# Performance work log

Measured on AMD Instinct MI355X. Metric: run time of the kernel, lower is better.

Reference implementation:

```python
import jax, jax.numpy as jnp
import numpy as np

B = 1024        # number of graphs in the batch
D = 256         # per-type node feature dim
DG = 128        # global (direct-cat) feature dim
N_ATOM = 65536
N_BOND = 131072
N_ITERS = 6


def _lstm_step(q_star, h, c, W_ih, W_hh, b_ih, b_hh):
    # torch LSTM gate order: i, f, g, o
    gates = q_star @ W_ih.T + b_ih + h @ W_hh.T + b_hh  # [B, 4D]
    i, f, g, o = jnp.split(gates, 4, axis=-1)
    c = jax.nn.sigmoid(f) * c + jax.nn.sigmoid(i) * jnp.tanh(g)
    h = jax.nn.sigmoid(o) * jnp.tanh(c)
    return h, c


def _set2set(feat, seg, W_ih, W_hh, b_ih, b_hh, n_iters, batch_size):
    d = feat.shape[1]
    h = jnp.zeros((batch_size, d), feat.dtype)
    c = jnp.zeros((batch_size, d), feat.dtype)
    q_star = jnp.zeros((batch_size, 2 * d), feat.dtype)
    for _ in range(n_iters):
        h, c = _lstm_step(q_star, h, c, W_ih, W_hh, b_ih, b_hh)
        q = h  # [B, D]
        # per-node attention logit: e_i = x_i . q_{seg(i)}
        e = jnp.sum(feat * q[seg], axis=-1)  # [N]
        # segment softmax (stable)
        m = jax.ops.segment_max(e, seg, num_segments=batch_size)
        ex = jnp.exp(e - m[seg])
        denom = jax.ops.segment_sum(ex, seg, num_segments=batch_size)
        alpha = ex / denom[seg]  # [N]
        # weighted readout per graph
        r = jax.ops.segment_sum(feat * alpha[:, None], seg, num_segments=batch_size)  # [B, D]
        q_star = jnp.concatenate([q, r], axis=-1)
    return q_star  # [B, 2D]


def setup_inputs() -> dict:
    key = jax.random.key(0)
    ks = jax.random.split(key, 12)
    s = 1.0 / np.sqrt(D)  # torch LSTM init range
    inp = {
        "feat_atom": jax.random.normal(ks[0], (N_ATOM, D), jnp.float32),
        "seg_atom": (jnp.arange(N_ATOM) // (N_ATOM // B)).astype(jnp.int32),
        "feat_bond": jax.random.normal(ks[1], (N_BOND, D), jnp.float32),
        "seg_bond": (jnp.arange(N_BOND) // (N_BOND // B)).astype(jnp.int32),
        "feat_global": jax.random.normal(ks[2], (B, DG), jnp.float32),
        "W_ih_atom": jax.random.uniform(ks[3], (4 * D, 2 * D), jnp.float32, -s, s),
        "W_hh_atom": jax.random.uniform(ks[4], (4 * D, D), jnp.float32, -s, s),
        "b_ih_atom": jax.random.uniform(ks[5], (4 * D,), jnp.float32, -s, s),
        "b_hh_atom": jax.random.uniform(ks[6], (4 * D,), jnp.float32, -s, s),
        "W_ih_bond": jax.random.uniform(ks[7], (4 * D, 2 * D), jnp.float32, -s, s),
        "W_hh_bond": jax.random.uniform(ks[8], (4 * D, D), jnp.float32, -s, s),
        "b_ih_bond": jax.random.uniform(ks[9], (4 * D,), jnp.float32, -s, s),
        "b_hh_bond": jax.random.uniform(ks[10], (4 * D,), jnp.float32, -s, s),
    }
    return inp


def reference(feat_atom, seg_atom, feat_bond, seg_bond, feat_global,
              W_ih_atom, W_hh_atom, b_ih_atom, b_hh_atom,
              W_ih_bond, W_hh_bond, b_ih_bond, b_hh_bond):
    qa = _set2set(feat_atom, seg_atom, W_ih_atom, W_hh_atom, b_ih_atom, b_hh_atom, N_ITERS, B)
    qb = _set2set(feat_bond, seg_bond, W_ih_bond, W_hh_bond, b_ih_bond, b_hh_bond, N_ITERS, B)
    return jnp.concatenate([qa, qb, feat_global], axis=-1)  # [B, 2D + 2D + DG]
```

## Files before the change

kernel.cpp:

```cpp
#include <hip/hip_runtime.h>
#include <stdint.h>

#define NGRAPH 1024
#define DFEAT  256
#define KATOM  64
#define KBOND  128

typedef __attribute__((ext_vector_type(4))) float accv_t;
typedef __attribute__((ext_vector_type(8))) short bfrag_t;
typedef __attribute__((ext_vector_type(4))) unsigned short upk4_t;
typedef __attribute__((ext_vector_type(8))) unsigned short upk8_t;
typedef __attribute__((ext_vector_type(4))) unsigned int u32x4;

__device__ __forceinline__ unsigned short f2bf(float f) {
    union { float f; unsigned int u; } v; v.f = f;
    return (unsigned short)((v.u + 0x7FFFu + ((v.u >> 16) & 1u)) >> 16);
}
__device__ __forceinline__ float sigm(float x) { return 1.0f / (1.0f + __expf(-x)); }
__device__ __forceinline__ float tanh_f(float x) {
    float e = __expf(2.0f * x);
    return 1.0f - 2.0f / (e + 1.0f);
}

__global__ __launch_bounds__(256) void k_cvt(
    const float* __restrict__ fA, const float* __restrict__ fB,
    unsigned int* __restrict__ oA, unsigned int* __restrict__ oB,
    float* __restrict__ scA, float* __restrict__ scB)
{
    int wid  = blockIdx.x * 4 + (threadIdx.x >> 6);
    int lane = threadIdx.x & 63;
    int grp  = lane >> 3;

    #pragma unroll 2
    for (int n = wid; n < 65536; n += 4096) {
        accv_t v = __builtin_nontemporal_load((const accv_t*)(fA + (size_t)n * 256) + lane);
        float m = fmaxf(fmaxf(fabsf(v[0]), fabsf(v[1])), fmaxf(fabsf(v[2]), fabsf(v[3])));
        m = fmaxf(m, __shfl_xor(m, 1));
        m = fmaxf(m, __shfl_xor(m, 2));
        m = fmaxf(m, __shfl_xor(m, 4));
        float inv = (m > 0.0f) ? 127.0f / m : 0.0f;
        int q0 = (int)rintf(v[0] * inv), q1 = (int)rintf(v[1] * inv);
        int q2 = (int)rintf(v[2] * inv), q3 = (int)rintf(v[3] * inv);
        oA[(size_t)n * 64 + lane] = (unsigned int)(q0 & 0xFF) | ((unsigned int)(q1 & 0xFF) << 8)
                                  | ((unsigned int)(q2 & 0xFF) << 16) | ((unsigned int)(q3 & 0xFF) << 24);
        if ((lane & 7) == 0) scA[(size_t)n * 8 + grp] = m * (1.0f / 127.0f);
    }
    #pragma unroll 2
    for (int n = wid; n < 131072; n += 4096) {
        accv_t v = __builtin_nontemporal_load((const accv_t*)(fB + (size_t)n * 256) + lane);
        float m = fmaxf(fmaxf(fabsf(v[0]), fabsf(v[1])), fmaxf(fabsf(v[2]), fabsf(v[3])));
        m = fmaxf(m, __shfl_xor(m, 1));
        m = fmaxf(m, __shfl_xor(m, 2));
        m = fmaxf(m, __shfl_xor(m, 4));
        float inv = (m > 0.0f) ? 127.0f / m : 0.0f;
        int q0 = (int)rintf(v[0] * inv), q1 = (int)rintf(v[1] * inv);
        int q2 = (int)rintf(v[2] * inv), q3 = (int)rintf(v[3] * inv);
        oB[(size_t)n * 64 + lane] = (unsigned int)(q0 & 0xFF) | ((unsigned int)(q1 & 0xFF) << 8)
                                  | ((unsigned int)(q2 & 0xFF) << 16) | ((unsigned int)(q3 & 0xFF) << 24);
        if ((lane & 7) == 0) scB[(size_t)n * 8 + grp] = m * (1.0f / 127.0f);
    }
}

__global__ __launch_bounds__(512) void k_prep(
    const float* __restrict__ WihA, const float* __restrict__ WhhA,
    const float* __restrict__ bihA, const float* __restrict__ bhhA,
    const float* __restrict__ WihB, const float* __restrict__ WhhB,
    const float* __restrict__ bihB, const float* __restrict__ bhhB,
    unsigned short* __restrict__ Wc, float* __restrict__ bsum)
{
    int bid = blockIdx.x;
    int set = bid >> 10;
    int n   = bid & 1023;
    int k   = threadIdx.x;
    const float* Wih = set ? WihB : WihA;
    const float* Whh = set ? WhhB : WhhA;
    float w = Wih[(size_t)n * 512 + k];
    if (k < 256) w += Whh[(size_t)n * 256 + k];
    Wc[((size_t)(set << 10) + n) * 512 + k] = f2bf(w);
    if (k == 0) {
        const float* bih = set ? bihB : bihA;
        const float* bhh = set ? bhhB : bhhA;
        bsum[(set << 10) + n] = bih[n] + bhh[n];
    }
}

__global__ __launch_bounds__(256) void k_gemm(
    const float* __restrict__ hr, const unsigned short* __restrict__ Wc,
    const float* __restrict__ bsum, float* __restrict__ gates)
{
    __shared__ unsigned short sA[64 * 40];
    __shared__ unsigned short sB[128 * 40];

    int set   = blockIdx.x >> 7;
    int qq    = blockIdx.x & 127;
    int mbase = (qq >> 3) * 64;
    int nbase = (qq & 7) * 128;
    int t     = threadIdx.x;
    int lane  = t & 63;
    int w     = t >> 6;
    int wrow  = (w >> 1) * 32;
    int wcol  = (w & 1) * 64;
    int l15   = lane & 15;
    int khalf = (lane >> 4) * 8;

    const float* A           = hr + (size_t)(set << 10) * 512;
    const unsigned short* Bm = Wc + (size_t)(set << 10) * 512;

    accv_t acc[2][4];
    #pragma unroll
    for (int i = 0; i < 2; ++i)
        #pragma unroll
        for (int j = 0; j < 4; ++j)
            acc[i][j] = (accv_t){0.f, 0.f, 0.f, 0.f};

    for (int k0 = 0; k0 < 512; k0 += 32) {
        #pragma unroll
        for (int i = 0; i < 2; ++i) {
            int idx4 = t + 256 * i;
            int row  = idx4 >> 3;
            int kc   = (idx4 & 7) * 4;
            const float4 a = *(const float4*)&A[(size_t)(mbase + row) * 512 + k0 + kc];
            upk4_t u;
            u[0] = f2bf(a.x); u[1] = f2bf(a.y); u[2] = f2bf(a.z); u[3] = f2bf(a.w);
            *(upk4_t*)&sA[row * 40 + kc] = u;
        }
        #pragma unroll
        for (int i = 0; i < 2; ++i) {
            int idx8 = t + 256 * i;
            int row  = idx8 >> 2;
            int kc   = (idx8 & 3) * 8;
            *(upk8_t*)&sB[row * 40 + kc] =
                *(const upk8_t*)&Bm[(size_t)(nbase + row) * 512 + k0 + kc];
        }
        __syncthreads();

        bfrag_t a_f[2], b_f[4];
        #pragma unroll
        for (int i = 0; i < 2; ++i)
            a_f[i] = *(const bfrag_t*)&sA[(wrow + i * 16 + l15) * 40 + khalf];
        #pragma unroll
        for (int j = 0; j < 4; ++j)
            b_f[j] = *(const bfrag_t*)&sB[(wcol + j * 16 + l15) * 40 + khalf];
        #pragma unroll
        for (int i = 0; i < 2; ++i)
            #pragma unroll
            for (int j = 0; j < 4; ++j)
                acc[i][j] = __builtin_amdgcn_mfma_f32_16x16x32_bf16(a_f[i], b_f[j], acc[i][j], 0, 0, 0);
        __syncthreads();
    }

    int r4 = (lane >> 4) * 4;
    #pragma unroll
    for (int i = 0; i < 2; ++i) {
        #pragma unroll
        for (int j = 0; j < 4; ++j) {
            int col  = nbase + wcol + j * 16 + l15;
            float bs = bsum[(set << 10) + col];
            #pragma unroll
            for (int v = 0; v < 4; ++v) {
                int row = mbase + wrow + i * 16 + r4 + v;
                gates[((size_t)(set << 10) + row) * 1024 + col] = acc[i][j][v] + bs;
            }
        }
    }
}

template <int MODE, bool LAST>
__global__ __launch_bounds__(256) void k_attn(
    const float* __restrict__ featA, const float* __restrict__ featB,
    const unsigned int* __restrict__ i8A, const unsigned int* __restrict__ i8B,
    const float* __restrict__ scA, const float* __restrict__ scB,
    const float* __restrict__ gates, const float* __restrict__ bsum,
    float* __restrict__ hr, float* __restrict__ cst,
    const float* __restrict__ fgp, float* __restrict__ outp, int iter)
{
    __shared__ float qv[256];
    __shared__ float sw_s[16], cw_s[16];
    __shared__ float racc_s[16][260];

    int bid = blockIdx.x;
    int set = (bid < 1024) ? 1 : 0;
    int b   = bid & 1023;
    int K   = set ? KBOND : KATOM;
    int t = threadIdx.x;
    size_t sb = (size_t)(set << 10) + b;
    size_t ob = (size_t)b * 1152 + (set ? 512 : 0);

    {
        int d = t;
        float gi, gf, gg, go, cold;
        if (iter == 0) {
            gi = bsum[(set << 10) + d];
            gf = bsum[(set << 10) + 256 + d];
            gg = bsum[(set << 10) + 512 + d];
            go = bsum[(set << 10) + 768 + d];
            cold = 0.0f;
        } else {
            const float* gp = gates + sb * 1024;
            gi = gp[d]; gf = gp[256 + d]; gg = gp[512 + d]; go = gp[768 + d];
            cold = cst[sb * 256 + d];
        }
        float cn = sigm(gf) * cold + sigm(gi) * tanh_f(gg);
        float h  = sigm(go) * tanh_f(cn);
        if (LAST) { outp[ob + d] = h; }
        else      { cst[sb * 256 + d] = cn; hr[sb * 512 + d] = h; }
        qv[d] = h;
    }
    __syncthreads();

    int lane = t & 63;
    int wv   = t >> 6;
    int g    = lane >> 4;
    int s    = lane & 15;
    int npw  = K >> 2;
    int nq   = npw >> 2;
    int node0 = wv * npw + g;
    float C = 0.0f, sacc = 0.0f;
    int pid = (wv << 2) | g;

    if (MODE == 1) {
        const unsigned int* fb = (set ? i8B : i8A)
                               + ((size_t)b * K + node0) * 64 + s * 4;
        const float* scp = (set ? scB : scA)
                         + ((size_t)b * K + node0) * 8 + (s >> 1);

        float qr[16];
        #pragma unroll
        for (int j = 0; j < 16; ++j) qr[j] = qv[s * 16 + j];
        float r[16];
        #pragma unroll
        for (int j = 0; j < 16; ++j) r[j] = 0.0f;

        #pragma unroll 4
        for (int qd = 0; qd < nq; ++qd) {
            u32x4 hx = *(const u32x4*)(fb + (size_t)qd * 256);
            float sc = scp[(size_t)qd * 32];
            float x[16];
            #pragma unroll
            for (int w4 = 0; w4 < 4; ++w4) {
                unsigned int u = hx[w4];
                x[w4 * 4 + 0] = (float)((int)(u << 24) >> 24);
                x[w4 * 4 + 1] = (float)((int)(u << 16) >> 24);
                x[w4 * 4 + 2] = (float)((int)(u << 8)  >> 24);
                x[w4 * 4 + 3] = (float)((int)u >> 24);
            }
            float e = 0.0f;
            #pragma unroll
            for (int j = 0; j < 16; ++j) e += x[j] * qr[j];
            e *= sc;
            e += __shfl_xor(e, 1);
            e += __shfl_xor(e, 2);
            e += __shfl_xor(e, 4);
            e += __shfl_xor(e, 8);
            float w = (qd == 0) ? 1.0f : __expf(e - C);
            if (qd == 0) C = e;
            sacc += w;
            float wl = w * sc;
            #pragma unroll
            for (int j = 0; j < 16; ++j) r[j] += wl * x[j];
        }
        #pragma unroll
        for (int j = 0; j < 16; j += 4)
            *(float4*)&racc_s[pid][s * 16 + j] = *(float4*)&r[j];
    } else {
        const float* feat = set ? featB : featA;
        const float* fb = feat + ((size_t)b * K + node0) * 256 + s * 4;
        float4 q0 = *(const float4*)&qv[s*4];
        float4 q1 = *(const float4*)&qv[64  + s*4];
        float4 q2 = *(const float4*)&qv[128 + s*4];
        float4 q3 = *(const float4*)&qv[192 + s*4];
        float4 r0 = make_float4(0.f,0.f,0.f,0.f), r1 = r0, r2 = r0, r3 = r0;
        #pragma unroll 2
        for (int qd = 0; qd < nq; ++qd) {
            const float* p = fb + (size_t)qd * 1024;
            float4 x0 = *(const float4*)(p);
            float4 x1 = *(const float4*)(p + 64);
            float4 x2 = *(const float4*)(p + 128);
            float4 x3 = *(const float4*)(p + 192);
            float e = x0.x*q0.x + x0.y*q0.y + x0.z*q0.z + x0.w*q0.w
                    + x1.x*q1.x + x1.y*q1.y + x1.z*q1.z + x1.w*q1.w
                    + x2.x*q2.x + x2.y*q2.y + x2.z*q2.z + x2.w*q2.w
                    + x3.x*q3.x + x3.y*q3.y + x3.z*q3.z + x3.w*q3.w;
            e += __shfl_xor(e, 1); e += __shfl_xor(e, 2);
            e += __shfl_xor(e, 4); e += __shfl_xor(e, 8);
            float w = (qd == 0) ? 1.0f : __expf(e - C);
            if (qd == 0) C = e;
            sacc += w;
            r0.x += w*x0.x; r0.y += w*x0.y; r0.z += w*x0.z; r0.w += w*x0.w;
            r1.x += w*x1.x; r1.y += w*x1.y; r1.z += w*x1.z; r1.w += w*x1.w;
            r2.x += w*x2.x; r2.y += w*x2.y; r2.z += w*x2.z; r2.w += w*x2.w;
            r3.x += w*x3.x; r3.y += w*x3.y; r3.z += w*x3.z; r3.w += w*x3.w;
        }
        *(float4*)&racc_s[pid][s*4]       = r0;
        *(float4*)&racc_s[pid][64  + s*4] = r1;
        *(float4*)&racc_s[pid][128 + s*4] = r2;
        *(float4*)&racc_s[pid][192 + s*4] = r3;
    }
    if (s == 0) { sw_s[pid] = sacc; cw_s[pid] = C; }
    __syncthreads();

    {
        float Cm = cw_s[0];
        #pragma unroll
        for (int p2 = 1; p2 < 16; ++p2) Cm = fmaxf(Cm, cw_s[p2]);
        float S = 0.0f, r = 0.0f;
        #pragma unroll
        for (int p2 = 0; p2 < 16; ++p2) {
            float f = __expf(cw_s[p2] - Cm);
            S += sw_s[p2] * f;
            r += racc_s[p2][t] * f;
        }
        float rv = r / S;
        if (LAST) {
            outp[ob + 256 + t] = rv;
            if (set && t < 128)
                outp[(size_t)b * 1152 + 1024 + t] = fgp[(size_t)b * 128 + t];
        } else {
            hr[sb * 512 + 256 + t] = rv;
        }
    }
}

__global__ __launch_bounds__(288) void k_out(
    const float* __restrict__ hr, const float* __restrict__ fg,
    float* __restrict__ out)
{
    int b  = blockIdx.x;
    int c4 = threadIdx.x * 4;
    float4 v;
    if (c4 < 512)       v = *(const float4*)&hr[(size_t)b * 512 + c4];
    else if (c4 < 1024) v = *(const float4*)&hr[(size_t)(1024 + b) * 512 + (c4 - 512)];
    else                v = *(const float4*)&fg[(size_t)b * 128 + (c4 - 1024)];
    *(float4*)&out[(size_t)b * 1152 + c4] = v;
}

extern "C" void kernel_launch(void* const* d_in, const int* in_sizes, int n_in,
                              void* d_out, int out_size, void* d_ws, size_t ws_size,
                              hipStream_t stream) {
    const float* feat_atom   = (const float*)d_in[0];
    const float* feat_bond   = (const float*)d_in[2];
    const float* feat_global = (const float*)d_in[4];
    const float* WihA = (const float*)d_in[5];
    const float* WhhA = (const float*)d_in[6];
    const float* bihA = (const float*)d_in[7];
    const float* bhhA = (const float*)d_in[8];
    const float* WihB = (const float*)d_in[9];
    const float* WhhB = (const float*)d_in[10];
    const float* bihB = (const float*)d_in[11];
    const float* bhhB = (const float*)d_in[12];
    float* out = (float*)d_out;

    char* ws = (char*)d_ws;
    unsigned short* Wc = (unsigned short*)(ws + 0);
    float* bsum  = (float*)(ws + 2097152);
    float* gates = (float*)(ws + 2105344);
    float* hr    = (float*)(ws + 10493952);
    float* cst   = (float*)(ws + 14688256);
    unsigned int* i8A = (unsigned int*)(ws + 16785408);
    unsigned int* i8B = (unsigned int*)(ws + 33562624);
    float* scA = (float*)(ws + 67117056);
    float* scB = (float*)(ws + 69214208);
    const size_t WS_NEED = 69214208 + 4194304;
    (void)in_sizes; (void)n_in; (void)out_size;

    bool i8 = (ws_size >= WS_NEED);

    k_prep<<<2048, 512, 0, stream>>>(WihA, WhhA, bihA, bhhA,
                                     WihB, WhhB, bihB, bhhB, Wc, bsum);
    if (i8) {
        k_cvt<<<1024, 256, 0, stream>>>(feat_atom, feat_bond, i8A, i8B, scA, scB);
        k_attn<1, false><<<2048, 256, 0, stream>>>(feat_atom, feat_bond, i8A, i8B,
                                                   scA, scB, gates, bsum, hr, cst,
                                                   feat_global, out, 0);
        for (int it = 1; it < 5; ++it) {
            k_gemm<<<256, 256, 0, stream>>>(hr, Wc, bsum, gates);
            k_attn<1, false><<<2048, 256, 0, stream>>>(feat_atom, feat_bond, i8A, i8B,
                                                       scA, scB, gates, bsum, hr, cst,
                                                       feat_global, out, it);
        }
        k_gemm<<<256, 256, 0, stream>>>(hr, Wc, bsum, gates);
        k_attn<1, true><<<2048, 256, 0, stream>>>(feat_atom, feat_bond, i8A, i8B,
                                                  scA, scB, gates, bsum, hr, cst,
                                                  feat_global, out, 5);
    } else {
        k_attn<2, false><<<2048, 256, 0, stream>>>(feat_atom, feat_bond, 0, 0, 0, 0,
                                                   gates, bsum, hr, cst,
                                                   feat_global, out, 0);
        for (int it = 1; it < 6; ++it) {
            k_gemm<<<256, 256, 0, stream>>>(hr, Wc, bsum, gates);
            k_attn<2, false><<<2048, 256, 0, stream>>>(feat_atom, feat_bond, 0, 0, 0, 0,
                                                       gates, bsum, hr, cst,
                                                       feat_global, out, it);
        }
        k_out<<<1024, 288, 0, stream>>>(hr, feat_global, out);
    }
}
```

Baseline: 223.3 us.

## Store hidden state and gates in bf16, fuse prep kernels, retile GEMM

The recurrent state buffer and the LSTM gate buffer are now stored as bf16 instead of fp32. This halves their traffic and removes the per-tile fp32-to-bf16 conversion inside the GEMM. The feature-quantization and weight-prep kernels are merged into one launch, and the GEMM uses 64x64 tiles with twice as many blocks to improve occupancy. The fallback path also drops its separate output kernel. The cost is extra rounding error on the gates and hidden state.

After: 185.6 us, median of 2. 16.9% less time.

```diff
diff --git a/kernel.cpp b/kernel.cpp
--- a/kernel.cpp
+++ b/kernel.cpp
@@ -16,135 +16,139 @@
     union { float f; unsigned int u; } v; v.f = f;
     return (unsigned short)((v.u + 0x7FFFu + ((v.u >> 16) & 1u)) >> 16);
 }
+__device__ __forceinline__ float bf2f(unsigned short h) {
+    union { unsigned int u; float f; } v; v.u = ((unsigned int)h) << 16;
+    return v.f;
+}
 __device__ __forceinline__ float sigm(float x) { return 1.0f / (1.0f + __expf(-x)); }
 __device__ __forceinline__ float tanh_f(float x) {
     float e = __expf(2.0f * x);
     return 1.0f - 2.0f / (e + 1.0f);
 }
-
-__global__ __launch_bounds__(256) void k_cvt(
+__device__ __forceinline__ unsigned int packq(float a, float b, float c, float d, float inv) {
+    int q0 = (int)rintf(a * inv), q1 = (int)rintf(b * inv);
+    int q2 = (int)rintf(c * inv), q3 = (int)rintf(d * inv);
+    return (unsigned int)(q0 & 0xFF) | ((unsigned int)(q1 & 0xFF) << 8)
+         | ((unsigned int)(q2 & 0xFF) << 16) | ((unsigned int)(q3 & 0xFF) << 24);
+}
+__device__ __forceinline__ void dec16(const unsigned int* h, float* x) {
+    #pragma unroll
+    for (int w4 = 0; w4 < 4; ++w4) {
+        unsigned int u = h[w4];
+        x[w4 * 4 + 0] = (float)((int)(u << 24) >> 24);
+        x[w4 * 4 + 1] = (float)((int)(u << 16) >> 24);
+        x[w4 * 4 + 2] = (float)((int)(u << 8)  >> 24);
+        x[w4 * 4 + 3] = (float)((int)u >> 24);
+    }
+}
+
+__global__ __launch_bounds__(256) void k_cvtprep(
     const float* __restrict__ fA, const float* __restrict__ fB,
     unsigned int* __restrict__ oA, unsigned int* __restrict__ oB,
-    float* __restrict__ scA, float* __restrict__ scB)
-{
-    int wid  = blockIdx.x * 4 + (threadIdx.x >> 6);
-    int lane = threadIdx.x & 63;
-    int grp  = lane >> 3;
-
-    #pragma unroll 2
-    for (int n = wid; n < 65536; n += 4096) {
-        accv_t v = __builtin_nontemporal_load((const accv_t*)(fA + (size_t)n * 256) + lane);
-        float m = fmaxf(fmaxf(fabsf(v[0]), fabsf(v[1])), fmaxf(fabsf(v[2]), fabsf(v[3])));
-        m = fmaxf(m, __shfl_xor(m, 1));
-        m = fmaxf(m, __shfl_xor(m, 2));
-        m = fmaxf(m, __shfl_xor(m, 4));
-        float inv = (m > 0.0f) ? 127.0f / m : 0.0f;
-        int q0 = (int)rintf(v[0] * inv), q1 = (int)rintf(v[1] * inv);
-        int q2 = (int)rintf(v[2] * inv), q3 = (int)rintf(v[3] * inv);
-        oA[(size_t)n * 64 + lane] = (unsigned int)(q0 & 0xFF) | ((unsigned int)(q1 & 0xFF) << 8)
-                                  | ((unsigned int)(q2 & 0xFF) << 16) | ((unsigned int)(q3 & 0xFF) << 24);
-        if ((lane & 7) == 0) scA[(size_t)n * 8 + grp] = m * (1.0f / 127.0f);
-    }
-    #pragma unroll 2
-    for (int n = wid; n < 131072; n += 4096) {
-        accv_t v = __builtin_nontemporal_load((const accv_t*)(fB + (size_t)n * 256) + lane);
-        float m = fmaxf(fmaxf(fabsf(v[0]), fabsf(v[1])), fmaxf(fabsf(v[2]), fabsf(v[3])));
-        m = fmaxf(m, __shfl_xor(m, 1));
-        m = fmaxf(m, __shfl_xor(m, 2));
-        m = fmaxf(m, __shfl_xor(m, 4));
-        float inv = (m > 0.0f) ? 127.0f / m : 0.0f;
-        int q0 = (int)rintf(v[0] * inv), q1 = (int)rintf(v[1] * inv);
-        int q2 = (int)rintf(v[2] * inv), q3 = (int)rintf(v[3] * inv);
-        oB[(size_t)n * 64 + lane] = (unsigned int)(q0 & 0xFF) | ((unsigned int)(q1 & 0xFF) << 8)
-                                  | ((unsigned int)(q2 & 0xFF) << 16) | ((unsigned int)(q3 & 0xFF) << 24);
-        if ((lane & 7) == 0) scB[(size_t)n * 8 + grp] = m * (1.0f / 127.0f);
-    }
-}
-
-__global__ __launch_bounds__(512) void k_prep(
+    float* __restrict__ scA, float* __restrict__ scB,
     const float* __restrict__ WihA, const float* __restrict__ WhhA,
     const float* __restrict__ bihA, const float* __restrict__ bhhA,
     const float* __restrict__ WihB, const float* __restrict__ WhhB,
     const float* __restrict__ bihB, const float* __restrict__ bhhB,
-    unsigned short* __restrict__ Wc, float* __restrict__ bsum)
+    unsigned short* __restrict__ Wc, float* __restrict__ bsum, int doquant)
 {
     int bid = blockIdx.x;
-    int set = bid >> 10;
-    int n   = bid & 1023;
-    int k   = threadIdx.x;
-    const float* Wih = set ? WihB : WihA;
-    const float* Whh = set ? WhhB : WhhA;
-    float w = Wih[(size_t)n * 512 + k];
-    if (k < 256) w += Whh[(size_t)n * 256 + k];
-    Wc[((size_t)(set << 10) + n) * 512 + k] = f2bf(w);
-    if (k == 0) {
-        const float* bih = set ? bihB : bihA;
-        const float* bhh = set ? bhhB : bhhA;
-        bsum[(set << 10) + n] = bih[n] + bhh[n];
+    if (bid < 1024) {
+        if (!doquant) return;
+        int wid  = bid * 4 + (threadIdx.x >> 6);
+        int lane = threadIdx.x & 63;
+        int grp  = lane >> 3;
+        #pragma unroll 2
+        for (int n = wid; n < 65536; n += 4096) {
+            accv_t v = __builtin_nontemporal_load((const accv_t*)(fA + (size_t)n * 256) + lane);
+            float m = fmaxf(fmaxf(fabsf(v[0]), fabsf(v[1])), fmaxf(fabsf(v[2]), fabsf(v[3])));
+            m = fmaxf(m, __shfl_xor(m, 1));
+            m = fmaxf(m, __shfl_xor(m, 2));
+            m = fmaxf(m, __shfl_xor(m, 4));
+            float inv = (m > 0.0f) ? 127.0f / m : 0.0f;
+            oA[(size_t)n * 64 + lane] = packq(v[0], v[1], v[2], v[3], inv);
+            if ((lane & 7) == 0) scA[(size_t)n * 8 + grp] = m * (1.0f / 127.0f);
+        }
+        #pragma unroll 2
+        for (int n = wid; n < 131072; n += 4096) {
+            accv_t v = __builtin_nontemporal_load((const accv_t*)(fB + (size_t)n * 256) + lane);
+            float m = fmaxf(fmaxf(fabsf(v[0]), fabsf(v[1])), fmaxf(fabsf(v[2]), fabsf(v[3])));
+            m = fmaxf(m, __shfl_xor(m, 1));
+            m = fmaxf(m, __shfl_xor(m, 2));
+            m = fmaxf(m, __shfl_xor(m, 4));
+            float inv = (m > 0.0f) ? 127.0f / m : 0.0f;
+            oB[(size_t)n * 64 + lane] = packq(v[0], v[1], v[2], v[3], inv);
+            if ((lane & 7) == 0) scB[(size_t)n * 8 + grp] = m * (1.0f / 127.0f);
+        }
+    } else {
+        int pid = bid - 1024;
+        int set = pid >> 10;
+        int n   = pid & 1023;
+        int k   = threadIdx.x;
+        const float* Wih = set ? WihB : WihA;
+        const float* Whh = set ? WhhB : WhhA;
+        float w1 = Wih[(size_t)n * 512 + k] + Whh[(size_t)n * 256 + k];
+        float w2 = Wih[(size_t)n * 512 + 256 + k];
+        size_t base = ((size_t)(set << 10) + n) * 512;
+        Wc[base + k]       = f2bf(w1);
+        Wc[base + 256 + k] = f2bf(w2);
+        if (k == 0) {
+            const float* bih = set ? bihB : bihA;
+            const float* bhh = set ? bhhB : bhhA;
+            bsum[(set << 10) + n] = bih[n] + bhh[n];
+        }
     }
 }
 
 __global__ __launch_bounds__(256) void k_gemm(
-    const float* __restrict__ hr, const unsigned short* __restrict__ Wc,
-    const float* __restrict__ bsum, float* __restrict__ gates)
+    const unsigned short* __restrict__ hrb, const unsigned short* __restrict__ Wc,
+    const float* __restrict__ bsum, unsigned short* __restrict__ gates)
 {
     __shared__ unsigned short sA[64 * 40];
-    __shared__ unsigned short sB[128 * 40];
-
-    int set   = blockIdx.x >> 7;
-    int qq    = blockIdx.x & 127;
-    int mbase = (qq >> 3) * 64;
-    int nbase = (qq & 7) * 128;
+    __shared__ unsigned short sB[64 * 40];
+
+    int set   = blockIdx.x >> 8;
+    int qq    = blockIdx.x & 255;
+    int mbase = (qq >> 4) * 64;
+    int nbase = (qq & 15) * 64;
     int t     = threadIdx.x;
     int lane  = t & 63;
     int w     = t >> 6;
     int wrow  = (w >> 1) * 32;
-    int wcol  = (w & 1) * 64;
+    int wcol  = (w & 1) * 32;
     int l15   = lane & 15;
     int khalf = (lane >> 4) * 8;
 
-    const float* A           = hr + (size_t)(set << 10) * 512;
-    const unsigned short* Bm = Wc + (size_t)(set << 10) * 512;
-
-    accv_t acc[2][4];
+    const unsigned short* Am = hrb + (size_t)(set << 10) * 512;
+    const unsigned short* Bm = Wc  + (size_t)(set << 10) * 512;
+
+    accv_t acc[2][2];
     #pragma unroll
     for (int i = 0; i < 2; ++i)
         #pragma unroll
-        for (int j = 0; j < 4; ++j)
+        for (int j = 0; j < 2; ++j)
             acc[i][j] = (accv_t){0.f, 0.f, 0.f, 0.f};
 
+    int srow = t >> 2;
+    int skc  = (t & 3) * 8;
     for (int k0 = 0; k0 < 512; k0 += 32) {
-        #pragma unroll
-        for (int i = 0; i < 2; ++i) {
-            int idx4 = t + 256 * i;
-            int row  = idx4 >> 3;
-            int kc   = (idx4 & 7) * 4;
-            const float4 a = *(const float4*)&A[(size_t)(mbase + row) * 512 + k0 + kc];
-            upk4_t u;
-            u[0] = f2bf(a.x); u[1] = f2bf(a.y); u[2] = f2bf(a.z); u[3] = f2bf(a.w);
-            *(upk4_t*)&sA[row * 40 + kc] = u;
-        }
-        #pragma unroll
-        for (int i = 0; i < 2; ++i) {
-            int idx8 = t + 256 * i;
-            int row  = idx8 >> 2;
-            int kc   = (idx8 & 3) * 8;
-            *(upk8_t*)&sB[row * 40 + kc] =
-                *(const upk8_t*)&Bm[(size_t)(nbase + row) * 512 + k0 + kc];
-        }
+        *(upk8_t*)&sA[srow * 40 + skc] =
+            *(const upk8_t*)&Am[(size_t)(mbase + srow) * 512 + k0 + skc];
+        *(upk8_t*)&sB[srow * 40 + skc] =
+            *(const upk8_t*)&Bm[(size_t)(nbase + srow) * 512 + k0 + skc];
         __syncthreads();
 
-        bfrag_t a_f[2], b_f[4];
+        bfrag_t a_f[2], b_f[2];
         #pragma unroll
         for (int i = 0; i < 2; ++i)
             a_f[i] = *(const bfrag_t*)&sA[(wrow + i * 16 + l15) * 40 + khalf];
         #pragma unroll
-        for (int j = 0; j < 4; ++j)
+        for (int j = 0; j < 2; ++j)
             b_f[j] = *(const bfrag_t*)&sB[(wcol + j * 16 + l15) * 40 + khalf];
         #pragma unroll
         for (int i = 0; i < 2; ++i)
             #pragma unroll
-            for (int j = 0; j < 4; ++j)
+            for (int j = 0; j < 2; ++j)
                 acc[i][j] = __builtin_amdgcn_mfma_f32_16x16x32_bf16(a_f[i], b_f[j], acc[i][j], 0, 0, 0);
         __syncthreads();
     }
@@ -153,13 +157,14 @@
     #pragma unroll
     for (int i = 0; i < 2; ++i) {
         #pragma unroll
-        for (int j = 0; j < 4; ++j) {
+        for (int j = 0; j < 2; ++j) {
             int col  = nbase + wcol + j * 16 + l15;
             float bs = bsum[(set << 10) + col];
             #pragma unroll
-            for (int v = 0; v < 4; ++v) {
-                int row = mbase + wrow + i * 16 + r4 + v;
-                gates[((size_t)(set << 10) + row) * 1024 + col] = acc[i][j][v] + bs;
+            for (int v = 0; v < 2; ++v) {
+                int row0 = mbase + wrow + i * 16 + r4 + 2 * v;
+                gates[((size_t)(set << 10) + row0) * 1024 + col]     = f2bf(acc[i][j][2 * v] + bs);
+                gates[((size_t)(set << 10) + row0 + 1) * 1024 + col] = f2bf(acc[i][j][2 * v + 1] + bs);
             }
         }
     }
@@ -170,8 +175,8 @@
     const float* __restrict__ featA, const float* __restrict__ featB,
     const unsigned int* __restrict__ i8A, const unsigned int* __restrict__ i8B,
     const float* __restrict__ scA, const float* __restrict__ scB,
-    const float* __restrict__ gates, const float* __restrict__ bsum,
-    float* __restrict__ hr, float* __restrict__ cst,
+    const unsigned short* __restrict__ gates, const float* __restrict__ bsum,
+    unsigned short* __restrict__ hrb, float* __restrict__ cst,
     const float* __restrict__ fgp, float* __restrict__ outp, int iter)
 {
     __shared__ float qv[256];
@@ -196,14 +201,15 @@
             go = bsum[(set << 10) + 768 + d];
             cold = 0.0f;
         } else {
-            const float* gp = gates + sb * 1024;
-            gi = gp[d]; gf = gp[256 + d]; gg = gp[512 + d]; go = gp[768 + d];
+            const unsigned short* gp = gates + sb * 1024;
+            gi = bf2f(gp[d]); gf = bf2f(gp[256 + d]);
+            gg = bf2f(gp[512 + d]); go = bf2f(gp[768 + d]);
             cold = cst[sb * 256 + d];
         }
         float cn = sigm(gf) * cold + sigm(gi) * tanh_f(gg);
         float h  = sigm(go) * tanh_f(cn);
         if (LAST) { outp[ob + d] = h; }
-        else      { cst[sb * 256 + d] = cn; hr[sb * 512 + d] = h; }
+        else      { cst[sb * 256 + d] = cn; hrb[sb * 512 + d] = f2bf(h); }
         qv[d] = h;
     }
     __syncthreads();
@@ -236,14 +242,7 @@
             u32x4 hx = *(const u32x4*)(fb + (size_t)qd * 256);
             float sc = scp[(size_t)qd * 32];
             float x[16];
-            #pragma unroll
-            for (int w4 = 0; w4 < 4; ++w4) {
-                unsigned int u = hx[w4];
-                x[w4 * 4 + 0] = (float)((int)(u << 24) >> 24);
-                x[w4 * 4 + 1] = (float)((int)(u << 16) >> 24);
-                x[w4 * 4 + 2] = (float)((int)(u << 8)  >> 24);
-                x[w4 * 4 + 3] = (float)((int)u >> 24);
-            }
+            dec16((const unsigned int*)&hx, x);
             float e = 0.0f;
             #pragma unroll
             for (int j = 0; j < 16; ++j) e += x[j] * qr[j];
@@ -316,22 +315,9 @@
             if (set && t < 128)
                 outp[(size_t)b * 1152 + 1024 + t] = fgp[(size_t)b * 128 + t];
         } else {
-            hr[sb * 512 + 256 + t] = rv;
-        }
-    }
-}
-
-__global__ __launch_bounds__(288) void k_out(
-    const float* __restrict__ hr, const float* __restrict__ fg,
-    float* __restrict__ out)
-{
-    int b  = blockIdx.x;
-    int c4 = threadIdx.x * 4;
-    float4 v;
-    if (c4 < 512)       v = *(const float4*)&hr[(size_t)b * 512 + c4];
-    else if (c4 < 1024) v = *(const float4*)&hr[(size_t)(1024 + b) * 512 + (c4 - 512)];
-    else                v = *(const float4*)&fg[(size_t)b * 128 + (c4 - 1024)];
-    *(float4*)&out[(size_t)b * 1152 + c4] = v;
+            hrb[sb * 512 + 256 + t] = f2bf(rv);
+        }
+    }
 }
 
 extern "C" void kernel_launch(void* const* d_in, const int* in_sizes, int n_in,
@@ -351,47 +337,51 @@
     float* out = (float*)d_out;
 
     char* ws = (char*)d_ws;
-    unsigned short* Wc = (unsigned short*)(ws + 0);
-    float* bsum  = (float*)(ws + 2097152);
-    float* gates = (float*)(ws + 2105344);
-    float* hr    = (float*)(ws + 10493952);
-    float* cst   = (float*)(ws + 14688256);
-    unsigned int* i8A = (unsigned int*)(ws + 16785408);
-    unsigned int* i8B = (unsigned int*)(ws + 33562624);
-    float* scA = (float*)(ws + 67117056);
-    float* scB = (float*)(ws + 69214208);
-    const size_t WS_NEED = 69214208 + 4194304;
+    unsigned short* Wc    = (unsigned short*)(ws + 0);
+    float*          bsum  = (float*)(ws + 2097152);
+    unsigned short* gates = (unsigned short*)(ws + 2105344);
+    unsigned short* hrb   = (unsigned short*)(ws + 6299648);
+    float*          cst   = (float*)(ws + 8396800);
+    unsigned int*   i8A   = (unsigned int*)(ws + 10493952);
+    unsigned int*   i8B   = (unsigned int*)(ws + 27271168);
+    float*          scA   = (float*)(ws + 60825600);
+    float*          scB   = (float*)(ws + 62922752);
+    const size_t WS_NEED = 62922752 + 4194304;
     (void)in_sizes; (void)n_in; (void)out_size;
 
     bool i8 = (ws_size >= WS_NEED);
 
-    k_prep<<<2048, 512, 0, stream>>>(WihA, WhhA, bihA, bhhA,
-                                     WihB, WhhB, bihB, bhhB, Wc, bsum);
+    k_cvtprep<<<3072, 256, 0, stream>>>(feat_atom, feat_bond, i8A, i8B, scA, scB,
+                                        WihA, WhhA, bihA, bhhA,
+                                        WihB, WhhB, bihB, bhhB,
+                                        Wc, bsum, i8 ? 1 : 0);
     if (i8) {
-        k_cvt<<<1024, 256, 0, stream>>>(feat_atom, feat_bond, i8A, i8B, scA, scB);
         k_attn<1, false><<<2048, 256, 0, stream>>>(feat_atom, feat_bond, i8A, i8B,
-                                                   scA, scB, gates, bsum, hr, cst,
+                                                   scA, scB, gates, bsum, hrb, cst,
                                                    feat_global, out, 0);
         for (int it = 1; it < 5; ++it) {
-            k_gemm<<<256, 256, 0, stream>>>(hr, Wc, bsum, gates);
+            k_gemm<<<512, 256, 0, stream>>>(hrb, Wc, bsum, gates);
             k_attn<1, false><<<2048, 256, 0, stream>>>(feat_atom, feat_bond, i8A, i8B,
-                                                       scA, scB, gates, bsum, hr, cst,
+                                                       scA, scB, gates, bsum, hrb, cst,
                                                        feat_global, out, it);
         }
-        k_gemm<<<256, 256, 0, stream>>>(hr, Wc, bsum, gates);
+        k_gemm<<<512, 256, 0, stream>>>(hrb, Wc, bsum, gates);
         k_attn<1, true><<<2048, 256, 0, stream>>>(feat_atom, feat_bond, i8A, i8B,
-                                                  scA, scB, gates, bsum, hr, cst,
+                                                  scA, scB, gates, bsum, hrb, cst,
                                                   feat_global, out, 5);
     } else {
         k_attn<2, false><<<2048, 256, 0, stream>>>(feat_atom, feat_bond, 0, 0, 0, 0,
-                                                   gates, bsum, hr, cst,
+                                                   gates, bsum, hrb, cst,
                                                    feat_global, out, 0);
-        for (int it = 1; it < 6; ++it) {
-            k_gemm<<<256, 256, 0, stream>>>(hr, Wc, bsum, gates);
+        for (int it = 1; it < 5; ++it) {
+            k_gemm<<<512, 256, 0, stream>>>(hrb, Wc, bsum, gates);
             k_attn<2, false><<<2048, 256, 0, stream>>>(feat_atom, feat_bond, 0, 0, 0, 0,
-                                                       gates, bsum, hr, cst,
+                                                       gates, bsum, hrb, cst,
                                                        feat_global, out, it);
         }
-        k_out<<<1024, 288, 0, stream>>>(hr, feat_global, out);
-    }
-}
+        k_gemm<<<512, 256, 0, stream>>>(hrb, Wc, bsum, gates);
+        k_attn<2, true><<<2048, 256, 0, stream>>>(feat_atom, feat_bond, 0, 0, 0, 0,
+                                                  gates, bsum, hrb, cst,
+                                                  feat_global, out, 5);
+    }
+}
```
